# Kernel tuning notes

Hardware: AMD Instinct MI355X
Metric: run time of the kernel (lower is better)

Reference implementation:

```python
import jax, jax.numpy as jnp
import numpy as np
import math

D_MODEL, HEADS, KQ = 1024, 16, 64
B, S = 2, 2048

def setup_inputs() -> dict:
    key = jax.random.key(0)
    k1, k2, k3, k4, k5 = jax.random.split(key, 5)
    scale = D_MODEL ** (-0.5)
    return {
        "x_BSE": jax.random.normal(k1, (B, S, D_MODEL), dtype=jnp.float32),
        "w_q": jax.random.normal(k2, (D_MODEL, HEADS, KQ), dtype=jnp.float32) * scale,
        "w_k": jax.random.normal(k3, (D_MODEL, HEADS, KQ), dtype=jnp.float32) * scale,
        "w_v": jax.random.normal(k4, (D_MODEL, HEADS, KQ), dtype=jnp.float32) * scale,
        "w_o": jax.random.normal(k5, (D_MODEL, HEADS, KQ), dtype=jnp.float32) * scale,
    }

def reference(x_BSE, w_q, w_k, w_v, w_o):
    # QKV projections (self-attention: memory = x)
    q_BSHK = jnp.einsum('BSE,EHK->BSHK', x_BSE, w_q)
    k_BMHK = jnp.einsum('BSE,EHK->BSHK', x_BSE, w_k)
    v_BMHK = jnp.einsum('BSE,EHK->BSHK', x_BSE, w_v)
    logits_BSHM = jnp.einsum('BSHK,BMHK->BSHM', q_BSHK, k_BMHK) / math.sqrt(KQ)
    # causal (diagonal) mask: query position >= memory position
    Sdim, Mdim = logits_BSHM.shape[1], logits_BSHM.shape[3]
    qpos = jnp.arange(Sdim)[:, None]          # [S,1]
    mpos = jnp.arange(Mdim)[None, :]          # [1,M]
    mask_SM = jnp.where(qpos >= mpos, 0.0, -jnp.inf).astype(logits_BSHM.dtype)
    logits_BSHM = logits_BSHM + mask_SM[None, :, None, :]
    probs_BSHM = jax.nn.softmax(logits_BSHM, axis=3)
    out_BSHK = jnp.einsum('BSHM,BMHK->BSHK', probs_BSHM, v_BMHK)
    return jnp.einsum('BSHK,EHK->BSE', out_BSHK, w_o)
```

## Files before the change

kernel.cpp:

```cpp
#include <hip/hip_runtime.h>
#include <hip/hip_bf16.h>

typedef __attribute__((ext_vector_type(4)))  float f32x4;
typedef __attribute__((ext_vector_type(16))) float f32x16;
typedef __attribute__((ext_vector_type(8)))  short short8;
typedef __attribute__((ext_vector_type(4)))  short short4v;

__device__ __forceinline__ short f2bf(float f) {
  union { float f; unsigned u; } x; x.f = f;
  unsigned r = (x.u + 0x7FFFu + ((x.u >> 16) & 1u)) >> 16;
  return (short)r;
}
__device__ __forceinline__ unsigned cvtpk(float lo, float hi) {
  unsigned r;
  asm("v_cvt_pk_bf16_f32 %0, %1, %2" : "=v"(r) : "v"(lo), "v"(hi));
  return r;
}

__global__ __launch_bounds__(256) void k_cast(const float* __restrict__ in,
                                              short* __restrict__ out, int n4) {
  int i = blockIdx.x * 256 + threadIdx.x;
  if (i >= n4) return;
  f32x4 v = ((const f32x4*)in)[i];
  short4v s;
  s[0] = f2bf(v[0]); s[1] = f2bf(v[1]); s[2] = f2bf(v[2]); s[3] = f2bf(v[3]);
  ((short4v*)out)[i] = s;
}

__global__ __launch_bounds__(256) void k_pack(const float* __restrict__ wq,
                                              const float* __restrict__ wk,
                                              const float* __restrict__ wv,
                                              short* __restrict__ WT) {
  int nt = blockIdx.x, et = blockIdx.y, sel = blockIdx.z;
  const float* w = sel == 0 ? wq : (sel == 1 ? wk : wv);
  __shared__ float tile[64][65];
  int tid = threadIdx.x;
  int cl = tid & 63, rw = tid >> 6;
#pragma unroll
  for (int j = 0; j < 16; ++j) {
    int el = j * 4 + rw;
    tile[el][cl] = w[(size_t)(et * 64 + el) * 1024 + nt * 64 + cl];
  }
  __syncthreads();
#pragma unroll
  for (int j = 0; j < 16; ++j) {
    int nl = j * 4 + rw;
    int n = sel * 1024 + nt * 64 + nl;
    WT[(size_t)n * 1024 + et * 64 + cl] = f2bf(tile[cl][nl]);
  }
}

template <int EPI>
__global__ __launch_bounds__(256) void k_gemm(const short* __restrict__ A,
                                              const short* __restrict__ B,
                                              short* __restrict__ Qo, short* __restrict__ Ko,
                                              short* __restrict__ Vo, float* __restrict__ out,
                                              int M, int N, int K) {
  __shared__ short As[128][40];
  __shared__ short Bs[128][40];
  int tid = threadIdx.x;
  int bm = blockIdx.y * 128, bn = blockIdx.x * 128;
  int wid = tid >> 6, lane = tid & 63;
  int wm = (wid >> 1) * 64, wn = (wid & 1) * 64;
  int lg = lane >> 4, lr = lane & 15;
  f32x4 acc[4][4] = {};

  int sr = tid >> 2, sc = tid & 3;
  const short* Ar0 = A + (size_t)(bm + sr) * K;
  const short* Ar1 = A + (size_t)(bm + sr + 64) * K;
  const short* Br0 = B + (size_t)(bn + sr) * K;
  const short* Br1 = B + (size_t)(bn + sr + 64) * K;

  short8 pa0 = *(const short8*)&Ar0[sc * 8];
  short8 pa1 = *(const short8*)&Ar1[sc * 8];
  short8 pb0 = *(const short8*)&Br0[sc * 8];
  short8 pb1 = *(const short8*)&Br1[sc * 8];

  int nk = K >> 5;
  for (int kt = 0; kt < nk; ++kt) {
    __syncthreads();
    *(short8*)&As[sr][sc * 8] = pa0;
    *(short8*)&As[sr + 64][sc * 8] = pa1;
    *(short8*)&Bs[sr][sc * 8] = pb0;
    *(short8*)&Bs[sr + 64][sc * 8] = pb1;
    if (kt + 1 < nk) {
      int ko = (kt + 1) * 32;
      pa0 = *(const short8*)&Ar0[ko + sc * 8];
      pa1 = *(const short8*)&Ar1[ko + sc * 8];
      pb0 = *(const short8*)&Br0[ko + sc * 8];
      pb1 = *(const short8*)&Br1[ko + sc * 8];
    }
    __syncthreads();
    short8 af[4], bf_[4];
#pragma unroll
    for (int mt = 0; mt < 4; ++mt)
      af[mt] = *(const short8*)&As[wm + mt * 16 + lr][lg * 8];
#pragma unroll
    for (int ntl = 0; ntl < 4; ++ntl)
      bf_[ntl] = *(const short8*)&Bs[wn + ntl * 16 + lr][lg * 8];
#pragma unroll
    for (int mt = 0; mt < 4; ++mt)
#pragma unroll
      for (int ntl = 0; ntl < 4; ++ntl)
        acc[mt][ntl] = __builtin_amdgcn_mfma_f32_16x16x32_bf16(af[mt], bf_[ntl], acc[mt][ntl], 0, 0, 0);
  }

#pragma unroll
  for (int mt = 0; mt < 4; ++mt)
#pragma unroll
    for (int ntl = 0; ntl < 4; ++ntl)
#pragma unroll
      for (int rr = 0; rr < 4; ++rr) {
        int m = bm + wm + mt * 16 + lg * 4 + rr;
        int n = bn + wn + ntl * 16 + lr;
        float val = acc[mt][ntl][rr];
        if (EPI == 0) {
          int b = m >> 11, s = m & 2047;
          int sel = n >> 10, hk = n & 1023;
          int h = hk >> 6, kd = hk & 63;
          if (sel == 0) Qo[((size_t)(b * 16 + h) * 2048 + s) * 64 + kd] = f2bf(val * 0.18033688011112042f);
          else if (sel == 1) Ko[((size_t)(b * 16 + h) * 2048 + s) * 64 + kd] = f2bf(val);
          else Vo[((size_t)(b * 16 + h) * 64 + kd) * 2048 + s] = f2bf(val);
        } else {
          out[(size_t)m * 1024 + n] = val;
        }
      }
}

__global__ __launch_bounds__(128, 2) void k_attn(const short* __restrict__ Q,
                                                 const short* __restrict__ K,
                                                 const short* __restrict__ VT,
                                                 short* __restrict__ O) {
  const int S = 2048;
  int bh = blockIdx.x;
  int g = 31 - blockIdx.y;

  int tid = threadIdx.x;
  int wid = tid >> 6, lane = tid & 63;
  int hi = lane >> 5, ln = lane & 31;
  int qw = 2 * g + wid;
  int q_g = qw * 32 + ln;
  int npair = g + 1;

  __shared__ short Ks[2][2][32][64];
  __shared__ short Vs[2][2][64][32];

  const short* Qb = Q + (size_t)bh * S * 64;
  const short* Kb = K + (size_t)bh * S * 64;
  const short* Vb = VT + (size_t)bh * 64 * S;

  short8 qf[4];
#pragma unroll
  for (int ds = 0; ds < 4; ++ds)
    qf[ds] = *(const short8*)&Qb[(size_t)q_g * 64 + ds * 16 + hi * 8];

  int kr = tid >> 2, kcb = tid & 3;
  int vd = tid >> 1, vcb = tid & 1;
  const short* kgp = Kb + (size_t)kr * 64;
  const short* vgp = Vb + (size_t)vd * S;

  short8 ka0 = *(const short8*)&kgp[kcb * 8];
  short8 ka1 = *(const short8*)&kgp[(kcb + 4) * 8];
  short8 kb0 = *(const short8*)&kgp[2048 + kcb * 8];
  short8 kb1 = *(const short8*)&kgp[2048 + (kcb + 4) * 8];
  short8 va0 = *(const short8*)&vgp[vcb * 8];
  short8 va1 = *(const short8*)&vgp[(vcb + 2) * 8];
  short8 vb0 = *(const short8*)&vgp[32 + vcb * 8];
  short8 vb1 = *(const short8*)&vgp[32 + (vcb + 2) * 8];

  f32x16 acoA = {}, acoB = {};
  float l = 0.f;

  for (int p = 0; p < npair; ++p) {
    int pb = p & 1;
    *(short8*)&Ks[pb][0][kr][(kcb ^ (kr & 7)) * 8]       = ka0;
    *(short8*)&Ks[pb][0][kr][((kcb + 4) ^ (kr & 7)) * 8] = ka1;
    *(short8*)&Ks[pb][1][kr][(kcb ^ (kr & 7)) * 8]       = kb0;
    *(short8*)&Ks[pb][1][kr][((kcb + 4) ^ (kr & 7)) * 8] = kb1;
    *(short8*)&Vs[pb][0][vd][(vcb ^ (vd & 3)) * 8]       = va0;
    *(short8*)&Vs[pb][0][vd][((vcb + 2) ^ (vd & 3)) * 8] = va1;
    *(short8*)&Vs[pb][1][vd][(vcb ^ (vd & 3)) * 8]       = vb0;
    *(short8*)&Vs[pb][1][vd][((vcb + 2) ^ (vd & 3)) * 8] = vb1;
    if (p + 1 < npair) {
      size_t ko0 = (size_t)(2 * p + 2) * 2048, ko1 = (size_t)(2 * p + 3) * 2048;
      size_t vo0 = (size_t)(2 * p + 2) * 32,   vo1 = (size_t)(2 * p + 3) * 32;
      ka0 = *(const short8*)&kgp[ko0 + kcb * 8];
      ka1 = *(const short8*)&kgp[ko0 + (kcb + 4) * 8];
      kb0 = *(const short8*)&kgp[ko1 + kcb * 8];
      kb1 = *(const short8*)&kgp[ko1 + (kcb + 4) * 8];
      va0 = *(const short8*)&vgp[vo0 + vcb * 8];
      va1 = *(const short8*)&vgp[vo0 + (vcb + 2) * 8];
      vb0 = *(const short8*)&vgp[vo1 + vcb * 8];
      vb1 = *(const short8*)&vgp[vo1 + (vcb + 2) * 8];
    }
    __syncthreads();

    int t0 = 2 * p, t1 = 2 * p + 1;

    short8 kc00 = *(const short8*)&Ks[pb][0][ln][((0 + hi) ^ (ln & 7)) * 8];
    short8 kc01 = *(const short8*)&Ks[pb][0][ln][((2 + hi) ^ (ln & 7)) * 8];
    short8 kc02 = *(const short8*)&Ks[pb][0][ln][((4 + hi) ^ (ln & 7)) * 8];
    short8 kc03 = *(const short8*)&Ks[pb][0][ln][((6 + hi) ^ (ln & 7)) * 8];
    short8 kc10 = *(const short8*)&Ks[pb][1][ln][((0 + hi) ^ (ln & 7)) * 8];
    short8 kc11 = *(const short8*)&Ks[pb][1][ln][((2 + hi) ^ (ln & 7)) * 8];
    short8 kc12 = *(const short8*)&Ks[pb][1][ln][((4 + hi) ^ (ln & 7)) * 8];
    short8 kc13 = *(const short8*)&Ks[pb][1][ln][((6 + hi) ^ (ln & 7)) * 8];

    f32x16 sa0 = {}, sa1 = {};
    __builtin_amdgcn_s_setprio(1);
    sa0 = __builtin_amdgcn_mfma_f32_32x32x16_bf16(kc00, qf[0], sa0, 0, 0, 0);
    sa1 = __builtin_amdgcn_mfma_f32_32x32x16_bf16(kc10, qf[0], sa1, 0, 0, 0);
    sa0 = __builtin_amdgcn_mfma_f32_32x32x16_bf16(kc01, qf[1], sa0, 0, 0, 0);
    sa1 = __builtin_amdgcn_mfma_f32_32x32x16_bf16(kc11, qf[1], sa1, 0, 0, 0);
    sa0 = __builtin_amdgcn_mfma_f32_32x32x16_bf16(kc02, qf[2], sa0, 0, 0, 0);
    sa1 = __builtin_amdgcn_mfma_f32_32x32x16_bf16(kc12, qf[2], sa1, 0, 0, 0);
    sa0 = __builtin_amdgcn_mfma_f32_32x32x16_bf16(kc03, qf[3], sa0, 0, 0, 0);
    sa1 = __builtin_amdgcn_mfma_f32_32x32x16_bf16(kc13, qf[3], sa1, 0, 0, 0);
    __builtin_amdgcn_s_setprio(0);

    if (t0 >= qw) {
#pragma unroll
      for (int r = 0; r < 16; ++r) {
        int kv_g = t0 * 32 + (r & 3) + 8 * (r >> 2) + 4 * hi;
        if (kv_g > q_g) sa0[r] = -1e30f;
      }
    }
    if (t1 >= qw) {
#pragma unroll
      for (int r = 0; r < 16; ++r) {
        int kv_g = t1 * 32 + (r & 3) + 8 * (r >> 2) + 4 * hi;
        if (kv_g > q_g) sa1[r] = -1e30f;
      }
    }

    float p0[16], p1[16];
#pragma unroll
    for (int r = 0; r < 16; ++r) p0[r] = exp2f(sa0[r]);
#pragma unroll
    for (int r = 0; r < 16; ++r) p1[r] = exp2f(sa1[r]);
    {
      float s00 = (p0[0] + p0[1]) + (p0[2] + p0[3]);
      float s01 = (p0[4] + p0[5]) + (p0[6] + p0[7]);
      float s02 = (p0[8] + p0[9]) + (p0[10] + p0[11]);
      float s03 = (p0[12] + p0[13]) + (p0[14] + p0[15]);
      float s10 = (p1[0] + p1[1]) + (p1[2] + p1[3]);
      float s11 = (p1[4] + p1[5]) + (p1[6] + p1[7]);
      float s12 = (p1[8] + p1[9]) + (p1[10] + p1[11]);
      float s13 = (p1[12] + p1[13]) + (p1[14] + p1[15]);
      l += ((s00 + s01) + (s02 + s03)) + ((s10 + s11) + (s12 + s13));
    }

    {
      short8 v00 = *(const short8*)&Vs[pb][0][ln][((0 + hi) ^ (ln & 3)) * 8];
      short8 v01 = *(const short8*)&Vs[pb][0][ln][((2 + hi) ^ (ln & 3)) * 8];
      short8 v10 = *(const short8*)&Vs[pb][0][32 + ln][((0 + hi) ^ (ln & 3)) * 8];
      short8 v11 = *(const short8*)&Vs[pb][0][32 + ln][((2 + hi) ^ (ln & 3)) * 8];
#pragma unroll
      for (int s = 0; s < 2; ++s) {
        unsigned c0 = cvtpk(p0[8 * s + 0], p0[8 * s + 1]);
        unsigned c1 = cvtpk(p0[8 * s + 2], p0[8 * s + 3]);
        unsigned c2 = cvtpk(p0[8 * s + 4], p0[8 * s + 5]);
        unsigned c3 = cvtpk(p0[8 * s + 6], p0[8 * s + 7]);
        unsigned pc0 = (unsigned)__shfl_xor((int)c0, 32);
        unsigned pc1 = (unsigned)__shfl_xor((int)c1, 32);
        unsigned pc2 = (unsigned)__shfl_xor((int)c2, 32);
        unsigned pc3 = (unsigned)__shfl_xor((int)c3, 32);
        union { unsigned u[4]; short8 v; } pbv;
        pbv.u[0] = hi ? pc2 : c0;
        pbv.u[1] = hi ? pc3 : c1;
        pbv.u[2] = hi ? c2 : pc0;
        pbv.u[3] = hi ? c3 : pc1;
        __builtin_amdgcn_s_setprio(1);
        if (s == 0) {
          acoA = __builtin_amdgcn_mfma_f32_32x32x16_bf16(v00, pbv.v, acoA, 0, 0, 0);
          acoB = __builtin_amdgcn_mfma_f32_32x32x16_bf16(v10, pbv.v, acoB, 0, 0, 0);
        } else {
          acoA = __builtin_amdgcn_mfma_f32_32x32x16_bf16(v01, pbv.v, acoA, 0, 0, 0);
          acoB = __builtin_amdgcn_mfma_f32_32x32x16_bf16(v11, pbv.v, acoB, 0, 0, 0);
        }
        __builtin_amdgcn_s_setprio(0);
      }
    }
    {
      short8 v00 = *(const short8*)&Vs[pb][1][ln][((0 + hi) ^ (ln & 3)) * 8];
      short8 v01 = *(const short8*)&Vs[pb][1][ln][((2 + hi) ^ (ln & 3)) * 8];
      short8 v10 = *(const short8*)&Vs[pb][1][32 + ln][((0 + hi) ^ (ln & 3)) * 8];
      short8 v11 = *(const short8*)&Vs[pb][1][32 + ln][((2 + hi) ^ (ln & 3)) * 8];
#pragma unroll
      for (int s = 0; s < 2; ++s) {
        unsigned c0 = cvtpk(p1[8 * s + 0], p1[8 * s + 1]);
        unsigned c1 = cvtpk(p1[8 * s + 2], p1[8 * s + 3]);
        unsigned c2 = cvtpk(p1[8 * s + 4], p1[8 * s + 5]);
        unsigned c3 = cvtpk(p1[8 * s + 6], p1[8 * s + 7]);
        unsigned pc0 = (unsigned)__shfl_xor((int)c0, 32);
        unsigned pc1 = (unsigned)__shfl_xor((int)c1, 32);
        unsigned pc2 = (unsigned)__shfl_xor((int)c2, 32);
        unsigned pc3 = (unsigned)__shfl_xor((int)c3, 32);
        union { unsigned u[4]; short8 v; } pbv;
        pbv.u[0] = hi ? pc2 : c0;
        pbv.u[1] = hi ? pc3 : c1;
        pbv.u[2] = hi ? c2 : pc0;
        pbv.u[3] = hi ? c3 : pc1;
        __builtin_amdgcn_s_setprio(1);
        if (s == 0) {
          acoA = __builtin_amdgcn_mfma_f32_32x32x16_bf16(v00, pbv.v, acoA, 0, 0, 0);
          acoB = __builtin_amdgcn_mfma_f32_32x32x16_bf16(v10, pbv.v, acoB, 0, 0, 0);
        } else {
          acoA = __builtin_amdgcn_mfma_f32_32x32x16_bf16(v01, pbv.v, acoA, 0, 0, 0);
          acoB = __builtin_amdgcn_mfma_f32_32x32x16_bf16(v11, pbv.v, acoB, 0, 0, 0);
        }
        __builtin_amdgcn_s_setprio(0);
      }
    }
  }

  l += __shfl_xor(l, 32);
  float rl = 1.f / l;
  int b = bh >> 4, h = bh & 15;
  size_t obase = ((size_t)b * 2048 + q_g) * 1024 + h * 64;
#pragma unroll
  for (int g4 = 0; g4 < 4; ++g4) {
    int d0 = 8 * g4 + 4 * hi;
    *(unsigned*)&O[obase + d0]          = cvtpk(acoA[4 * g4] * rl, acoA[4 * g4 + 1] * rl);
    *(unsigned*)&O[obase + d0 + 2]      = cvtpk(acoA[4 * g4 + 2] * rl, acoA[4 * g4 + 3] * rl);
    *(unsigned*)&O[obase + 32 + d0]     = cvtpk(acoB[4 * g4] * rl, acoB[4 * g4 + 1] * rl);
    *(unsigned*)&O[obase + 32 + d0 + 2] = cvtpk(acoB[4 * g4 + 2] * rl, acoB[4 * g4 + 3] * rl);
  }
}

extern "C" void kernel_launch(void* const* d_in, const int* in_sizes, int n_in,
                              void* d_out, int out_size, void* d_ws, size_t ws_size,
                              hipStream_t stream) {
  const float* x  = (const float*)d_in[0];
  const float* wq = (const float*)d_in[1];
  const float* wk = (const float*)d_in[2];
  const float* wv = (const float*)d_in[3];
  const float* wo = (const float*)d_in[4];
  float* out = (float*)d_out;
  char* ws = (char*)d_ws;

  short* x_bf  = (short*)(ws);
  short* WqkvT = (short*)(ws + ((size_t)8 << 20));
  short* wo_bf = (short*)(ws + ((size_t)14 << 20));
  short* Qb    = (short*)(ws + ((size_t)16 << 20));
  short* Kb    = (short*)(ws + ((size_t)24 << 20));
  short* Vt    = (short*)(ws + ((size_t)32 << 20));
  short* Ob    = (short*)(ws + ((size_t)40 << 20));

  k_cast<<<4096, 256, 0, stream>>>(x, x_bf, 1048576);
  k_cast<<<1024, 256, 0, stream>>>(wo, wo_bf, 262144);
  k_pack<<<dim3(16, 16, 3), 256, 0, stream>>>(wq, wk, wv, WqkvT);
  k_gemm<0><<<dim3(24, 32), 256, 0, stream>>>(x_bf, WqkvT, Qb, Kb, Vt, nullptr, 4096, 3072, 1024);
  k_attn<<<dim3(32, 32), 128, 0, stream>>>(Qb, Kb, Vt, Ob);
  k_gemm<1><<<dim3(8, 32), 256, 0, stream>>>(Ob, wo_bf, nullptr, nullptr, nullptr, out, 4096, 1024, 1024);
}
```

Measured before the change: 129.7 us.

## Stage attention K/V tiles with direct global-to-LDS loads and vectorize V epilogue

The attention kernel now uses global_load_lds to copy K and V tiles straight into shared memory, double-buffered, with a waitcnt and barrier at the end of each iteration. This replaces the register-staged loads followed by LDS stores. The aim is to save VGPRs and LDS-store instructions while keeping the next tile's load overlapped with compute. The projection GEMM epilogue also writes the transposed V output as a 4-element vector store. The risks are correctness of the per-wave LDS destination layout and the per-iteration vmcnt(0) wait, which could expose load latency.

```diff
diff --git a/kernel.cpp b/kernel.cpp
--- a/kernel.cpp
+++ b/kernel.cpp
@@ -15,6 +15,10 @@
   unsigned r;
   asm("v_cvt_pk_bf16_f32 %0, %1, %2" : "=v"(r) : "v"(lo), "v"(hi));
   return r;
+}
+__device__ __forceinline__ void gload16(const short* g, short* l) {
+  __builtin_amdgcn_global_load_lds((const __attribute__((address_space(1))) void*)g,
+                                   (__attribute__((address_space(3))) void*)l, 16, 0, 0);
 }
 
 __global__ __launch_bounds__(256) void k_cast(const float* __restrict__ in,
@@ -108,23 +112,34 @@
 #pragma unroll
   for (int mt = 0; mt < 4; ++mt)
 #pragma unroll
-    for (int ntl = 0; ntl < 4; ++ntl)
-#pragma unroll
-      for (int rr = 0; rr < 4; ++rr) {
-        int m = bm + wm + mt * 16 + lg * 4 + rr;
-        int n = bn + wn + ntl * 16 + lr;
-        float val = acc[mt][ntl][rr];
-        if (EPI == 0) {
-          int b = m >> 11, s = m & 2047;
-          int sel = n >> 10, hk = n & 1023;
-          int h = hk >> 6, kd = hk & 63;
-          if (sel == 0) Qo[((size_t)(b * 16 + h) * 2048 + s) * 64 + kd] = f2bf(val * 0.18033688011112042f);
-          else if (sel == 1) Ko[((size_t)(b * 16 + h) * 2048 + s) * 64 + kd] = f2bf(val);
-          else Vo[((size_t)(b * 16 + h) * 64 + kd) * 2048 + s] = f2bf(val);
+    for (int ntl = 0; ntl < 4; ++ntl) {
+      int m0 = bm + wm + mt * 16 + lg * 4;
+      int n = bn + wn + ntl * 16 + lr;
+      if (EPI == 0) {
+        int b = m0 >> 11, s0 = m0 & 2047;
+        int sel = n >> 10, hk = n & 1023;
+        int h = hk >> 6, kd = hk & 63;
+        if (sel == 0) {
+#pragma unroll
+          for (int rr = 0; rr < 4; ++rr)
+            Qo[((size_t)(b * 16 + h) * 2048 + s0 + rr) * 64 + kd] =
+                f2bf(acc[mt][ntl][rr] * 0.18033688011112042f);
+        } else if (sel == 1) {
+#pragma unroll
+          for (int rr = 0; rr < 4; ++rr)
+            Ko[((size_t)(b * 16 + h) * 2048 + s0 + rr) * 64 + kd] = f2bf(acc[mt][ntl][rr]);
         } else {
-          out[(size_t)m * 1024 + n] = val;
+          short4v v4;
+#pragma unroll
+          for (int rr = 0; rr < 4; ++rr) v4[rr] = f2bf(acc[mt][ntl][rr]);
+          *(short4v*)&Vo[((size_t)(b * 16 + h) * 64 + kd) * 2048 + s0] = v4;
         }
-      }
+      } else {
+#pragma unroll
+        for (int rr = 0; rr < 4; ++rr)
+          out[(size_t)(m0 + rr) * 1024 + n] = acc[mt][ntl][rr];
+      }
+    }
 }
 
 __global__ __launch_bounds__(128, 2) void k_attn(const short* __restrict__ Q,
@@ -142,8 +157,8 @@
   int q_g = qw * 32 + ln;
   int npair = g + 1;
 
-  __shared__ short Ks[2][2][32][64];
-  __shared__ short Vs[2][2][64][32];
+  __shared__ short Ks[2][2][32 * 64];
+  __shared__ short Vs[2][2][64 * 32];
 
   const short* Qb = Q + (size_t)bh * S * 64;
   const short* Kb = K + (size_t)bh * S * 64;
@@ -154,57 +169,56 @@
   for (int ds = 0; ds < 4; ++ds)
     qf[ds] = *(const short8*)&Qb[(size_t)q_g * 64 + ds * 16 + hi * 8];
 
-  int kr = tid >> 2, kcb = tid & 3;
-  int vd = tid >> 1, vcb = tid & 1;
-  const short* kgp = Kb + (size_t)kr * 64;
-  const short* vgp = Vb + (size_t)vd * S;
-
-  short8 ka0 = *(const short8*)&kgp[kcb * 8];
-  short8 ka1 = *(const short8*)&kgp[(kcb + 4) * 8];
-  short8 kb0 = *(const short8*)&kgp[2048 + kcb * 8];
-  short8 kb1 = *(const short8*)&kgp[2048 + (kcb + 4) * 8];
-  short8 va0 = *(const short8*)&vgp[vcb * 8];
-  short8 va1 = *(const short8*)&vgp[(vcb + 2) * 8];
-  short8 vb0 = *(const short8*)&vgp[32 + vcb * 8];
-  short8 vb1 = *(const short8*)&vgp[32 + (vcb + 2) * 8];
+  int ksr0 = wid * 8 + (lane >> 3);
+  int kc = lane & 7;
+  const short* kSrc0 = Kb + ksr0 * 64 + ((kc ^ (ksr0 & 7)) * 8);
+  int ksr1 = ksr0 + 16;
+  const short* kSrc1 = Kb + ksr1 * 64 + ((kc ^ (ksr1 & 7)) * 8);
+  int vdr0 = wid * 16 + (lane >> 2);
+  int vc = lane & 3;
+  const short* vSrc0 = Vb + (size_t)vdr0 * S + ((vc ^ (vdr0 & 3)) * 8);
+  int vdr1 = vdr0 + 32;
+  const short* vSrc1 = Vb + (size_t)vdr1 * S + ((vc ^ (vdr1 & 3)) * 8);
 
   f32x16 acoA = {}, acoB = {};
   float l = 0.f;
 
+#define STAGE_PAIR(pbuf, t0)                                                    \
+  {                                                                             \
+    short* kd0 = &Ks[pbuf][0][0] + wid * 512;                                   \
+    short* kd1 = &Ks[pbuf][1][0] + wid * 512;                                   \
+    short* vdp0 = &Vs[pbuf][0][0] + wid * 512;                                  \
+    short* vdp1 = &Vs[pbuf][1][0] + wid * 512;                                  \
+    size_t ko = (size_t)(t0) * 2048;                                            \
+    size_t vo = (size_t)(t0) * 32;                                              \
+    gload16(kSrc0 + ko, kd0);                                                   \
+    gload16(kSrc1 + ko, kd0 + 1024);                                            \
+    gload16(kSrc0 + ko + 2048, kd1);                                            \
+    gload16(kSrc1 + ko + 2048, kd1 + 1024);                                     \
+    gload16(vSrc0 + vo, vdp0);                                                  \
+    gload16(vSrc1 + vo, vdp0 + 1024);                                           \
+    gload16(vSrc0 + vo + 32, vdp1);                                             \
+    gload16(vSrc1 + vo + 32, vdp1 + 1024);                                      \
+  }
+
+  STAGE_PAIR(0, 0)
+  asm volatile("s_waitcnt vmcnt(0)" ::: "memory");
+  __builtin_amdgcn_s_barrier();
+
   for (int p = 0; p < npair; ++p) {
     int pb = p & 1;
-    *(short8*)&Ks[pb][0][kr][(kcb ^ (kr & 7)) * 8]       = ka0;
-    *(short8*)&Ks[pb][0][kr][((kcb + 4) ^ (kr & 7)) * 8] = ka1;
-    *(short8*)&Ks[pb][1][kr][(kcb ^ (kr & 7)) * 8]       = kb0;
-    *(short8*)&Ks[pb][1][kr][((kcb + 4) ^ (kr & 7)) * 8] = kb1;
-    *(short8*)&Vs[pb][0][vd][(vcb ^ (vd & 3)) * 8]       = va0;
-    *(short8*)&Vs[pb][0][vd][((vcb + 2) ^ (vd & 3)) * 8] = va1;
-    *(short8*)&Vs[pb][1][vd][(vcb ^ (vd & 3)) * 8]       = vb0;
-    *(short8*)&Vs[pb][1][vd][((vcb + 2) ^ (vd & 3)) * 8] = vb1;
-    if (p + 1 < npair) {
-      size_t ko0 = (size_t)(2 * p + 2) * 2048, ko1 = (size_t)(2 * p + 3) * 2048;
-      size_t vo0 = (size_t)(2 * p + 2) * 32,   vo1 = (size_t)(2 * p + 3) * 32;
-      ka0 = *(const short8*)&kgp[ko0 + kcb * 8];
-      ka1 = *(const short8*)&kgp[ko0 + (kcb + 4) * 8];
-      kb0 = *(const short8*)&kgp[ko1 + kcb * 8];
-      kb1 = *(const short8*)&kgp[ko1 + (kcb + 4) * 8];
-      va0 = *(const short8*)&vgp[vo0 + vcb * 8];
-      va1 = *(const short8*)&vgp[vo0 + (vcb + 2) * 8];
-      vb0 = *(const short8*)&vgp[vo1 + vcb * 8];
-      vb1 = *(const short8*)&vgp[vo1 + (vcb + 2) * 8];
-    }
-    __syncthreads();
+    if (p + 1 < npair) STAGE_PAIR(pb ^ 1, 2 * p + 2)
 
     int t0 = 2 * p, t1 = 2 * p + 1;
 
-    short8 kc00 = *(const short8*)&Ks[pb][0][ln][((0 + hi) ^ (ln & 7)) * 8];
-    short8 kc01 = *(const short8*)&Ks[pb][0][ln][((2 + hi) ^ (ln & 7)) * 8];
-    short8 kc02 = *(const short8*)&Ks[pb][0][ln][((4 + hi) ^ (ln & 7)) * 8];
-    short8 kc03 = *(const short8*)&Ks[pb][0][ln][((6 + hi) ^ (ln & 7)) * 8];
-    short8 kc10 = *(const short8*)&Ks[pb][1][ln][((0 + hi) ^ (ln & 7)) * 8];
-    short8 kc11 = *(const short8*)&Ks[pb][1][ln][((2 + hi) ^ (ln & 7)) * 8];
-    short8 kc12 = *(const short8*)&Ks[pb][1][ln][((4 + hi) ^ (ln & 7)) * 8];
-    short8 kc13 = *(const short8*)&Ks[pb][1][ln][((6 + hi) ^ (ln & 7)) * 8];
+    short8 kc00 = *(const short8*)&Ks[pb][0][ln * 64 + (((0 + hi) ^ (ln & 7)) * 8)];
+    short8 kc01 = *(const short8*)&Ks[pb][0][ln * 64 + (((2 + hi) ^ (ln & 7)) * 8)];
+    short8 kc02 = *(const short8*)&Ks[pb][0][ln * 64 + (((4 + hi) ^ (ln & 7)) * 8)];
+    short8 kc03 = *(const short8*)&Ks[pb][0][ln * 64 + (((6 + hi) ^ (ln & 7)) * 8)];
+    short8 kc10 = *(const short8*)&Ks[pb][1][ln * 64 + (((0 + hi) ^ (ln & 7)) * 8)];
+    short8 kc11 = *(const short8*)&Ks[pb][1][ln * 64 + (((2 + hi) ^ (ln & 7)) * 8)];
+    short8 kc12 = *(const short8*)&Ks[pb][1][ln * 64 + (((4 + hi) ^ (ln & 7)) * 8)];
+    short8 kc13 = *(const short8*)&Ks[pb][1][ln * 64 + (((6 + hi) ^ (ln & 7)) * 8)];
 
     f32x16 sa0 = {}, sa1 = {};
     __builtin_amdgcn_s_setprio(1);
@@ -251,10 +265,10 @@
     }
 
     {
-      short8 v00 = *(const short8*)&Vs[pb][0][ln][((0 + hi) ^ (ln & 3)) * 8];
-      short8 v01 = *(const short8*)&Vs[pb][0][ln][((2 + hi) ^ (ln & 3)) * 8];
-      short8 v10 = *(const short8*)&Vs[pb][0][32 + ln][((0 + hi) ^ (ln & 3)) * 8];
-      short8 v11 = *(const short8*)&Vs[pb][0][32 + ln][((2 + hi) ^ (ln & 3)) * 8];
+      short8 v00 = *(const short8*)&Vs[pb][0][ln * 32 + (((0 + hi) ^ (ln & 3)) * 8)];
+      short8 v01 = *(const short8*)&Vs[pb][0][ln * 32 + (((2 + hi) ^ (ln & 3)) * 8)];
+      short8 v10 = *(const short8*)&Vs[pb][0][(32 + ln) * 32 + (((0 + hi) ^ (ln & 3)) * 8)];
+      short8 v11 = *(const short8*)&Vs[pb][0][(32 + ln) * 32 + (((2 + hi) ^ (ln & 3)) * 8)];
 #pragma unroll
       for (int s = 0; s < 2; ++s) {
         unsigned c0 = cvtpk(p0[8 * s + 0], p0[8 * s + 1]);
@@ -282,10 +296,10 @@
       }
     }
     {
-      short8 v00 = *(const short8*)&Vs[pb][1][ln][((0 + hi) ^ (ln & 3)) * 8];
-      short8 v01 = *(const short8*)&Vs[pb][1][ln][((2 + hi) ^ (ln & 3)) * 8];
-      short8 v10 = *(const short8*)&Vs[pb][1][32 + ln][((0 + hi) ^ (ln & 3)) * 8];
-      short8 v11 = *(const short8*)&Vs[pb][1][32 + ln][((2 + hi) ^ (ln & 3)) * 8];
+      short8 v00 = *(const short8*)&Vs[pb][1][ln * 32 + (((0 + hi) ^ (ln & 3)) * 8)];
+      short8 v01 = *(const short8*)&Vs[pb][1][ln * 32 + (((2 + hi) ^ (ln & 3)) * 8)];
+      short8 v10 = *(const short8*)&Vs[pb][1][(32 + ln) * 32 + (((0 + hi) ^ (ln & 3)) * 8)];
+      short8 v11 = *(const short8*)&Vs[pb][1][(32 + ln) * 32 + (((2 + hi) ^ (ln & 3)) * 8)];
 #pragma unroll
       for (int s = 0; s < 2; ++s) {
         unsigned c0 = cvtpk(p1[8 * s + 0], p1[8 * s + 1]);
@@ -312,7 +326,11 @@
         __builtin_amdgcn_s_setprio(0);
       }
     }
-  }
+
+    asm volatile("s_waitcnt vmcnt(0)" ::: "memory");
+    __builtin_amdgcn_s_barrier();
+  }
+#undef STAGE_PAIR
 
   l += __shfl_xor(l, 32);
   float rl = 1.f / l;
```

Result: no change. 127.7 us (-1.5%).
